# Performance work log

Hardware: AMD Instinct MI355X
Metric: run time of the kernel (lower is better)

The kernel has to match this reference:

```python
import jax, jax.numpy as jnp
import numpy as np

KSIZE = 3
PAD = (KSIZE - 1) // 2
SIG = 0.3 * ((KSIZE - 1) * 0.5 - 1) + 0.8  # sigma_space == sigma_density == 0.8
INV2S2 = 1.0 / (2.0 * SIG * SIG)


def _gauss_space():
    c = KSIZE // 2
    xs = np.arange(KSIZE, dtype=np.float32)
    gx, gy = np.meshgrid(xs, xs, indexing='xy')
    w = np.exp(-(((gx - c) ** 2 + (gy - c) ** 2)) * INV2S2)
    w = w / w.sum()
    return jnp.asarray(w, dtype=jnp.float32)


def _patches(x):
    # x: [N,C,H,W] -> [N,C,H,W,k,k], zero padding (matches F.pad value=0)
    H, W = x.shape[-2], x.shape[-1]
    xp = jnp.pad(x, ((0, 0), (0, 0), (PAD, PAD), (PAD, PAD)))
    rows = []
    for i in range(KSIZE):
        cols = [xp[:, :, i:i + H, j:j + W] for j in range(KSIZE)]
        rows.append(jnp.stack(cols, axis=-1))
    return jnp.stack(rows, axis=-2)


def setup_inputs() -> dict:
    key = jax.random.key(0)
    k1, k2, k3 = jax.random.split(key, 3)
    B, V, C, H, W = 2, 4, 3, 512, 512
    depth = jax.random.uniform(k1, (B, V, 1, H, W), dtype=jnp.float32)
    color = jax.random.uniform(k2, (B, V, C, H, W), dtype=jnp.float32)
    mask = jax.random.uniform(k3, (B, V, 1, H, W), dtype=jnp.float32)
    return {"depth": depth, "color": color, "mask": mask}


def reference(depth, color, mask):
    B, V, C, H, W = color.shape
    d = depth.reshape(B * V, 1, H, W)
    m = mask.reshape(B * V, 1, H, W)
    c = color.reshape(B * V, C, H, W)

    dp = _patches(d)  # [N,1,H,W,k,k]
    cp = _patches(c)  # [N,C,H,W,k,k]
    mp = _patches(m)  # [N,1,H,W,k,k]

    # depth (density) gaussian weight, normalized per-pixel over the window
    wd = jnp.exp(-((dp - d[..., None, None]) ** 2) * INV2S2)
    wd = wd / wd.sum(axis=(-1, -2), keepdims=True)

    # color gaussian weight summed over channels, normalized per-pixel
    wc = jnp.exp(-((cp - c[..., None, None]) ** 2) * INV2S2).sum(axis=1, keepdims=True)
    wc = wc / wc.sum(axis=(-1, -2), keepdims=True)

    ws = _gauss_space().reshape(1, 1, 1, 1, KSIZE, KSIZE)

    w = wd * wc * ws * mp + 1e-7  # [N,1,H,W,k,k]
    out = (w * cp).sum(axis=(-1, -2)) / w.sum(axis=(-1, -2))  # [N,C,H,W]
    return out.reshape(B, V, C, H, W)
```

## Files before the change

kernel.cpp:

```cpp
#include <hip/hip_runtime.h>


constexpr int HH = 512;
constexpr int WW = 512;
constexpr int HW = HH * WW;

#define KEXP (-1.1271055f)
#define E2(x) __builtin_amdgcn_exp2f(x)
#define WS0f 0.2724967f
#define WS1f 0.1247577f
#define WS2f 0.0571180f

__global__ __launch_bounds__(256) void bilateral_v5(
    const float* __restrict__ depth,
    const float* __restrict__ color,
    const float* __restrict__ mask,
    float* __restrict__ out)
{
    const int lane = threadIdx.x & 63;
    const int wg   = blockIdx.x * 4 + (threadIdx.x >> 6);
    const int n    = wg >> 9;
    const int rem  = wg & 511;
    const int hp   = rem >> 1;
    const int half = rem & 1;
    const int rA   = hp * 2;
    const int c0   = half * 256 + lane * 4;

    const float* dptr = depth + (size_t)n * HW;
    const float* mptr = mask  + (size_t)n * HW;
    const float* xptr = color + (size_t)n * 3 * HW;
    const float* yptr = xptr + HW;
    const float* zptr = xptr + 2 * HW;

    const bool hasL = (c0 > 0);
    const bool hasR = (c0 < WW - 4);

    float AD[6], AM[6], AX[6], AY[6], AZ[6];
    float BD[6], BM[6], BX[6], BY[6], BZ[6];

#define LOADP(W, base, ro) do {                                              \
    const float4 _q = *reinterpret_cast<const float4*>((base) + (ro));       \
    W[1] = _q.x; W[2] = _q.y; W[3] = _q.z; W[4] = _q.w;                      \
    W[0] = hasL ? (base)[(ro) - 1] : 0.0f;                                   \
    W[5] = hasR ? (base)[(ro) + 4] : 0.0f;                                   \
} while (0)

#define LOADW(D_, M_, X_, Y_, Z_, r) do {                                    \
    const int _ro = (r) * WW + c0;                                           \
    LOADP(D_, dptr, _ro); LOADP(M_, mptr, _ro);                              \
    LOADP(X_, xptr, _ro); LOADP(Y_, yptr, _ro); LOADP(Z_, zptr, _ro);        \
} while (0)

    float aSwd[4], aSwc[4], aSt[4], aS0[4], aS1[4], aS2[4];
    float bSwd[4], bSwc[4], bSt[4], bS0[4], bS1[4], bS2[4];
    #pragma unroll
    for (int i = 0; i < 4; ++i) {
        aSwd[i]=0.f; aSwc[i]=0.f; aSt[i]=0.f; aS0[i]=0.f; aS1[i]=0.f; aS2[i]=0.f;
        bSwd[i]=0.f; bSwc[i]=0.f; bSt[i]=0.f; bS0[i]=0.f; bS1[i]=0.f; bS2[i]=0.f;
    }

#define HPASS(D_, M_, X_, Y_, Z_, Swd, Swc, St, S0, S1, S2) do {             \
    float hwd[5], hwc[5];                                                    \
    _Pragma("unroll") for (int j = 0; j < 5; ++j) {                          \
        const float dd = D_[j] - D_[j + 1];                                  \
        hwd[j] = E2(KEXP * dd * dd);                                         \
        const float f0 = X_[j] - X_[j + 1];                                  \
        const float f1 = Y_[j] - Y_[j + 1];                                  \
        const float f2 = Z_[j] - Z_[j + 1];                                  \
        hwc[j] = E2(KEXP * f0 * f0) + E2(KEXP * f1 * f1)                     \
               + E2(KEXP * f2 * f2);                                         \
    }                                                                        \
    _Pragma("unroll") for (int i = 0; i < 4; ++i) {                          \
        const int ci = i + 1;                                                \
        { const float t = (3.0f * WS0f) * M_[ci];      \
          Swd[i] += 1.0f; Swc[i] += 3.0f; St[i] += t;                        \
          S0[i] += t * X_[ci]; S1[i] += t * Y_[ci]; S2[i] += t * Z_[ci]; }   \
        { const float t = hwd[i] * hwc[i] * WS1f * M_[i];          \
          Swd[i] += hwd[i]; Swc[i] += hwc[i]; St[i] += t;                    \
          S0[i] += t * X_[i]; S1[i] += t * Y_[i]; S2[i] += t * Z_[i]; }      \
        { const float t = hwd[i+1] * hwc[i+1] * WS1f * M_[i+2];    \
          Swd[i] += hwd[i+1]; Swc[i] += hwc[i+1]; St[i] += t;                \
          S0[i] += t * X_[i+2]; S1[i] += t * Y_[i+2]; S2[i] += t * Z_[i+2];} \
    }                                                                        \
} while (0)

    LOADW(AD, AM, AX, AY, AZ, rA);
    LOADW(BD, BM, BX, BY, BZ, rA + 1);

    float cdA[4], cxA[4], cyA[4], czA[4];
    float cdB[4], cxB[4], cyB[4], czB[4];
    #pragma unroll
    for (int i = 0; i < 4; ++i) {
        cdA[i] = AD[i+1]; cxA[i] = AX[i+1]; cyA[i] = AY[i+1]; czA[i] = AZ[i+1];
        cdB[i] = BD[i+1]; cxB[i] = BX[i+1]; cyB[i] = BY[i+1]; czB[i] = BZ[i+1];
    }

    HPASS(AD, AM, AX, AY, AZ, aSwd, aSwc, aSt, aS0, aS1, aS2);
    HPASS(BD, BM, BX, BY, BZ, bSwd, bSwc, bSt, bS0, bS1, bS2);

    #pragma unroll
    for (int a = 0; a < 6; ++a) {
        #pragma unroll
        for (int db = -1; db <= 1; ++db) {
            const int bb = a + db;
            if (bb < 0 || bb > 5) continue;
            const bool useA = (a >= 1 && a <= 4);
            const bool useB = (bb >= 1 && bb <= 4);
            if (!useA && !useB) continue;
            const float dd = AD[a] - BD[bb];
            const float pwd = E2(KEXP * dd * dd);
            const float f0 = AX[a] - BX[bb];
            const float f1 = AY[a] - BY[bb];
            const float f2 = AZ[a] - BZ[bb];
            const float pwc = E2(KEXP * f0 * f0) + E2(KEXP * f1 * f1)
                            + E2(KEXP * f2 * f2);
            const float g = pwd * pwc;
            const float ws = (db == 0) ? WS1f : WS2f;
            if (useA) {
                const int i = a - 1;
                const float t = g * ws * BM[bb];
                aSwd[i] += pwd; aSwc[i] += pwc; aSt[i] += t;
                aS0[i] += t * BX[bb]; aS1[i] += t * BY[bb]; aS2[i] += t * BZ[bb];
            }
            if (useB) {
                const int i = bb - 1;
                const float t = g * ws * AM[a];
                bSwd[i] += pwd; bSwc[i] += pwc; bSt[i] += t;
                bS0[i] += t * AX[a]; bS1[i] += t * AY[a]; bS2[i] += t * AZ[a];
            }
        }
    }

#define SIDE(TD, TM, TX, TY, TZ, cd, cx, cy, cz, Swd, Swc, St, S0, S1, S2) do { \
    _Pragma("unroll") for (int i = 0; i < 4; ++i) {                          \
        _Pragma("unroll") for (int dj = 0; dj < 3; ++dj) {                   \
            const int c = i + dj;                                            \
            const float dd = TD[c] - cd[i];                                  \
            const float wd = E2(KEXP * dd * dd);                             \
            const float f0 = TX[c] - cx[i];                                  \
            const float f1 = TY[c] - cy[i];                                  \
            const float f2 = TZ[c] - cz[i];                                  \
            const float wc = E2(KEXP * f0 * f0) + E2(KEXP * f1 * f1)         \
                           + E2(KEXP * f2 * f2);                             \
            const float ws = (dj == 1) ? WS1f : WS2f;                        \
            const float t = wd * wc * ws * TM[c];                            \
            Swd[i] += wd; Swc[i] += wc; St[i] += t;                          \
            S0[i] += t * TX[c]; S1[i] += t * TY[c]; S2[i] += t * TZ[c];      \
        }                                                                    \
    }                                                                        \
} while (0)

    if (hp > 0) {
        LOADW(AD, AM, AX, AY, AZ, rA - 1);
        SIDE(AD, AM, AX, AY, AZ, cdA, cxA, cyA, czA,
             aSwd, aSwc, aSt, aS0, aS1, aS2);
    }
    if (hp < 255) {
        LOADW(BD, BM, BX, BY, BZ, rA + 2);
        SIDE(BD, BM, BX, BY, BZ, cdB, cxB, cyB, czB,
             bSwd, bSwc, bSt, bS0, bS1, bS2);
    }

    float oa0[4], oa1[4], oa2[4], ob0[4], ob1[4], ob2[4];
    #pragma unroll
    for (int i = 0; i < 4; ++i) {
        const float invA = __builtin_amdgcn_rcpf(aSt[i] + 9e-7f * aSwd[i] * aSwc[i]);
        oa0[i] = aS0[i] * invA; oa1[i] = aS1[i] * invA; oa2[i] = aS2[i] * invA;
        const float invB = __builtin_amdgcn_rcpf(bSt[i] + 9e-7f * bSwd[i] * bSwc[i]);
        ob0[i] = bS0[i] * invB; ob1[i] = bS1[i] * invB; ob2[i] = bS2[i] * invB;
    }

    float* po = out + (size_t)n * 3 * HW + rA * WW + c0;
    *reinterpret_cast<float4*>(po)               = make_float4(oa0[0], oa0[1], oa0[2], oa0[3]);
    *reinterpret_cast<float4*>(po + HW)          = make_float4(oa1[0], oa1[1], oa1[2], oa1[3]);
    *reinterpret_cast<float4*>(po + 2 * HW)      = make_float4(oa2[0], oa2[1], oa2[2], oa2[3]);
    *reinterpret_cast<float4*>(po + WW)          = make_float4(ob0[0], ob0[1], ob0[2], ob0[3]);
    *reinterpret_cast<float4*>(po + WW + HW)     = make_float4(ob1[0], ob1[1], ob1[2], ob1[3]);
    *reinterpret_cast<float4*>(po + WW + 2 * HW) = make_float4(ob2[0], ob2[1], ob2[2], ob2[3]);
}

extern "C" void kernel_launch(void* const* d_in, const int* in_sizes, int n_in,
                              void* d_out, int out_size, void* d_ws, size_t ws_size,
                              hipStream_t stream) {
    const float* depth = (const float*)d_in[0];
    const float* color = (const float*)d_in[1];
    const float* mask  = (const float*)d_in[2];
    float* out = (float*)d_out;

    bilateral_v5<<<1024, 256, 0, stream>>>(depth, color, mask, out);
}
```

Measured before the change: 26.15 us.

## Prefetch halo rows early and swizzle block order across XCDs

```diff
diff --git a/kernel.cpp b/kernel.cpp
--- a/kernel.cpp
+++ b/kernel.cpp
@@ -11,14 +11,16 @@
 #define WS1f 0.1247577f
 #define WS2f 0.0571180f
 
-__global__ __launch_bounds__(256) void bilateral_v5(
+__global__ __launch_bounds__(256) void bilateral_v6(
     const float* __restrict__ depth,
     const float* __restrict__ color,
     const float* __restrict__ mask,
     float* __restrict__ out)
 {
     const int lane = threadIdx.x & 63;
-    const int wg   = blockIdx.x * 4 + (threadIdx.x >> 6);
+    const int b    = blockIdx.x;
+    const int logical = (b & 7) * 128 + (b >> 3);
+    const int wg   = logical * 4 + (int)(threadIdx.x >> 6);
     const int n    = wg >> 9;
     const int rem  = wg & 511;
     const int hp   = rem >> 1;
@@ -37,6 +39,7 @@
 
     float AD[6], AM[6], AX[6], AY[6], AZ[6];
     float BD[6], BM[6], BX[6], BY[6], BZ[6];
+    float PD[6], PM[6], PX[6], PY[6], PZ[6];
 
 #define LOADP(W, base, ro) do {                                              \
     const float4 _q = *reinterpret_cast<const float4*>((base) + (ro));       \
@@ -84,19 +87,45 @@
     }                                                                        \
 } while (0)
 
+#define SIDE(TD, TM, TX, TY, TZ, RD, RX, RY, RZ, Swd, Swc, St, S0, S1, S2) do { \
+    _Pragma("unroll") for (int i = 0; i < 4; ++i) {                          \
+        const float cd = RD[i + 1];                                          \
+        const float cx = RX[i + 1];                                          \
+        const float cy = RY[i + 1];                                          \
+        const float cz = RZ[i + 1];                                          \
+        _Pragma("unroll") for (int dj = 0; dj < 3; ++dj) {                   \
+            const int c = i + dj;                                            \
+            const float dd = TD[c] - cd;                                     \
+            const float wd = E2(KEXP * dd * dd);                             \
+            const float f0 = TX[c] - cx;                                     \
+            const float f1 = TY[c] - cy;                                     \
+            const float f2 = TZ[c] - cz;                                     \
+            const float wc = E2(KEXP * f0 * f0) + E2(KEXP * f1 * f1)         \
+                           + E2(KEXP * f2 * f2);                             \
+            const float ws = (dj == 1) ? WS1f : WS2f;                        \
+            const float t = wd * wc * ws * TM[c];                            \
+            Swd[i] += wd; Swc[i] += wc; St[i] += t;                          \
+            S0[i] += t * TX[c]; S1[i] += t * TY[c]; S2[i] += t * TZ[c];      \
+        }                                                                    \
+    }                                                                        \
+} while (0)
+
+    const bool hasUp = (hp > 0);
+    const bool hasDn = (hp < 255);
+
     LOADW(AD, AM, AX, AY, AZ, rA);
     LOADW(BD, BM, BX, BY, BZ, rA + 1);
-
-    float cdA[4], cxA[4], cyA[4], czA[4];
-    float cdB[4], cxB[4], cyB[4], czB[4];
-    #pragma unroll
-    for (int i = 0; i < 4; ++i) {
-        cdA[i] = AD[i+1]; cxA[i] = AX[i+1]; cyA[i] = AY[i+1]; czA[i] = AZ[i+1];
-        cdB[i] = BD[i+1]; cxB[i] = BX[i+1]; cyB[i] = BY[i+1]; czB[i] = BZ[i+1];
-    }
+    if (hasUp) LOADW(PD, PM, PX, PY, PZ, rA - 1);
 
     HPASS(AD, AM, AX, AY, AZ, aSwd, aSwc, aSt, aS0, aS1, aS2);
     HPASS(BD, BM, BX, BY, BZ, bSwd, bSwc, bSt, bS0, bS1, bS2);
+
+    if (hasUp) {
+        SIDE(PD, PM, PX, PY, PZ, AD, AX, AY, AZ,
+             aSwd, aSwc, aSt, aS0, aS1, aS2);
+    }
+
+    if (hasDn) LOADW(PD, PM, PX, PY, PZ, rA + 2);
 
     #pragma unroll
     for (int a = 0; a < 6; ++a) {
@@ -131,33 +160,8 @@
         }
     }
 
-#define SIDE(TD, TM, TX, TY, TZ, cd, cx, cy, cz, Swd, Swc, St, S0, S1, S2) do { \
-    _Pragma("unroll") for (int i = 0; i < 4; ++i) {                          \
-        _Pragma("unroll") for (int dj = 0; dj < 3; ++dj) {                   \
-            const int c = i + dj;                                            \
-            const float dd = TD[c] - cd[i];                                  \
-            const float wd = E2(KEXP * dd * dd);                             \
-            const float f0 = TX[c] - cx[i];                                  \
-            const float f1 = TY[c] - cy[i];                                  \
-            const float f2 = TZ[c] - cz[i];                                  \
-            const float wc = E2(KEXP * f0 * f0) + E2(KEXP * f1 * f1)         \
-                           + E2(KEXP * f2 * f2);                             \
-            const float ws = (dj == 1) ? WS1f : WS2f;                        \
-            const float t = wd * wc * ws * TM[c];                            \
-            Swd[i] += wd; Swc[i] += wc; St[i] += t;                          \
-            S0[i] += t * TX[c]; S1[i] += t * TY[c]; S2[i] += t * TZ[c];      \
-        }                                                                    \
-    }                                                                        \
-} while (0)
-
-    if (hp > 0) {
-        LOADW(AD, AM, AX, AY, AZ, rA - 1);
-        SIDE(AD, AM, AX, AY, AZ, cdA, cxA, cyA, czA,
-             aSwd, aSwc, aSt, aS0, aS1, aS2);
-    }
-    if (hp < 255) {
-        LOADW(BD, BM, BX, BY, BZ, rA + 2);
-        SIDE(BD, BM, BX, BY, BZ, cdB, cxB, cyB, czB,
+    if (hasDn) {
+        SIDE(PD, PM, PX, PY, PZ, BD, BX, BY, BZ,
              bSwd, bSwc, bSt, bS0, bS1, bS2);
     }
 
@@ -187,5 +191,5 @@
     const float* mask  = (const float*)d_in[2];
     float* out = (float*)d_out;
 
-    bilateral_v5<<<1024, 256, 0, stream>>>(depth, color, mask, out);
+    bilateral_v6<<<1024, 256, 0, stream>>>(depth, color, mask, out);
 }
```

Result: slower. 27.36 us (+4.6%).
